# Optimization experiments

Measured on AMD Instinct MI355X. Metric: run time of the kernel, lower is better.

Reference implementation:

```python
import jax, jax.numpy as jnp
import numpy as np

NUM_HEADS = 16
NUM_GROUPS = 32  # min(C//4, 32) with C=1024
EPS = 1e-6       # flax GroupNorm default


def setup_inputs() -> dict:
    key = jax.random.key(0)
    ks = jax.random.split(key, 3)
    B, L, C = 2, 2048, 1024
    x = jax.random.normal(ks[0], (B, L, C), dtype=jnp.float32)
    gn_scale = jnp.ones((C,), jnp.float32)
    gn_bias = jnp.zeros((C,), jnp.float32)
    qkv_w = jax.random.normal(ks[1], (C, 3 * C), jnp.float32) * (C ** -0.5)
    qkv_b = jnp.zeros((3 * C,), jnp.float32)
    proj_w = jax.random.normal(ks[2], (C, C), jnp.float32) * 1e-5  # default_init(1e-10) ~ tiny
    proj_b = jnp.zeros((C,), jnp.float32)
    return {"x": x, "gn_scale": gn_scale, "gn_bias": gn_bias,
            "qkv_w": qkv_w, "qkv_b": qkv_b, "proj_w": proj_w, "proj_b": proj_b}


def reference(x, gn_scale, gn_bias, qkv_w, qkv_b, proj_w, proj_b):
    B, L, C = x.shape
    H = NUM_HEADS
    hd = C // H
    # GroupNorm over (L, channels-in-group)
    xg = x.reshape(B, L, NUM_GROUPS, C // NUM_GROUPS)
    mu = jnp.mean(xg, axis=(1, 3), keepdims=True)
    var = jnp.var(xg, axis=(1, 3), keepdims=True)
    xn = ((xg - mu) * jax.lax.rsqrt(var + EPS)).reshape(B, L, C)
    xn = xn * gn_scale + gn_bias
    # 1x1-conv QKV projection == dense
    qkv = xn @ qkv_w + qkv_b                       # [B, L, 3C]
    qkv = qkv.reshape(B, L, H, 3 * hd)             # interleaved per-head q|k|v
    q, k, v = jnp.split(qkv, 3, axis=-1)           # each [B, L, H, hd]
    scale = 1.0 / jnp.sqrt(hd)
    logits = jnp.einsum('btnh,bfnh->bnft', k, q * scale)  # [B, H, L, L]
    weights = jax.nn.softmax(logits, axis=-1)
    h = jnp.einsum('bnft,btnh->bfnh', weights, v).reshape(B, L, C)
    h = h @ proj_w + proj_b
    # CombineResidualSkip, project_skip=False
    return (x + h) / np.sqrt(2.0)
```

## Files before the change

kernel.cpp:

```cpp
#include <hip/hip_runtime.h>
#include <hip/hip_bf16.h>

typedef __hip_bfloat16 bf16;
typedef __attribute__((ext_vector_type(8))) __bf16 bf16x8;
typedef __attribute__((ext_vector_type(4))) float floatx4;

#define NB 2
#define NL 2048
#define NC 1024
#define NH 16
#define ND 64

__device__ __forceinline__ void async_copy16(void* lds, const void* g) {
  __builtin_amdgcn_global_load_lds(
      (__attribute__((address_space(1))) void*)(const_cast<void*>(g)),
      (__attribute__((address_space(3))) void*)(lds), 16, 0, 0);
}

__device__ __forceinline__ floatx4 mfma16(bf16x8 a, bf16x8 b, floatx4 c) {
  return __builtin_amdgcn_mfma_f32_16x16x32_bf16(a, b, c, 0, 0, 0);
}

__global__ __launch_bounds__(256) void gn_part_kernel(
    const float* __restrict__ x, float2* __restrict__ part) {
  int bg = blockIdx.x >> 3, sl = blockIdx.x & 7;
  int b = bg >> 5, g = bg & 31;
  const float* base = x + (size_t)b * NL * NC + (size_t)(sl * 256) * NC + g * 32;
  float s = 0.f, ss = 0.f;
  for (int vi = threadIdx.x; vi < 2048; vi += 256) {
    int l = vi >> 3, j = (vi & 7) * 4;
    float4 u = *(const float4*)(base + (size_t)l * NC + j);
    s += u.x + u.y + u.z + u.w;
    ss += u.x * u.x + u.y * u.y + u.z * u.z + u.w * u.w;
  }
  for (int off = 32; off; off >>= 1) {
    s += __shfl_down(s, off);
    ss += __shfl_down(ss, off);
  }
  __shared__ float rs[4], rss[4];
  int wave = threadIdx.x >> 6, lane = threadIdx.x & 63;
  if (lane == 0) { rs[wave] = s; rss[wave] = ss; }
  __syncthreads();
  if (threadIdx.x == 0) {
    part[blockIdx.x] = make_float2(rs[0] + rs[1] + rs[2] + rs[3],
                                   rss[0] + rss[1] + rss[2] + rss[3]);
  }
}

__global__ __launch_bounds__(256) void gn_apply_kernel(
    const float* __restrict__ x, const float2* __restrict__ part,
    const float* __restrict__ scale, const float* __restrict__ bias,
    bf16* __restrict__ xn) {
  size_t idx = (size_t)blockIdx.x * 256 + threadIdx.x;
  size_t e = idx * 8;
  int c = (int)(e & (NC - 1));
  int b = (int)(e >> 21);
  int bg = b * 32 + (c >> 5);
  float s = 0.f, ss = 0.f;
#pragma unroll
  for (int i = 0; i < 8; ++i) {
    float2 p = part[bg * 8 + i];
    s += p.x; ss += p.y;
  }
  float mean = s * (1.f / 65536.f);
  float var = ss * (1.f / 65536.f) - mean * mean;
  float rstd = rsqrtf(var + 1e-6f);
  float4 x0 = *(const float4*)(x + e);
  float4 x1 = *(const float4*)(x + e + 4);
  float4 s0 = *(const float4*)(scale + c);
  float4 s1 = *(const float4*)(scale + c + 4);
  float4 b0 = *(const float4*)(bias + c);
  float4 b1 = *(const float4*)(bias + c + 4);
  float xv[8] = {x0.x, x0.y, x0.z, x0.w, x1.x, x1.y, x1.z, x1.w};
  float sv[8] = {s0.x, s0.y, s0.z, s0.w, s1.x, s1.y, s1.z, s1.w};
  float bv[8] = {b0.x, b0.y, b0.z, b0.w, b1.x, b1.y, b1.z, b1.w};
  bf16 o[8];
#pragma unroll
  for (int k = 0; k < 8; ++k)
    o[k] = __float2bfloat16((xv[k] - mean) * rstd * sv[k] + bv[k]);
  *(uint4*)(xn + e) = *(const uint4*)o;
}

__global__ void transpose_f32_bf16(const float* __restrict__ in,
                                   bf16* __restrict__ out, int R, int C) {
  __shared__ float t[32][33];
  int c0 = blockIdx.x * 32, r0 = blockIdx.y * 32;
#pragma unroll
  for (int j = 0; j < 4; ++j)
    t[threadIdx.y + j * 8][threadIdx.x] =
        in[(size_t)(r0 + threadIdx.y + j * 8) * C + c0 + threadIdx.x];
  __syncthreads();
#pragma unroll
  for (int j = 0; j < 4; ++j)
    out[(size_t)(c0 + threadIdx.y + j * 8) * R + r0 + threadIdx.x] =
        __float2bfloat16(t[threadIdx.x][threadIdx.y + j * 8]);
}

template <int MODE, int NT>
__global__ __launch_bounds__(256) void gemm_kernel(
    const bf16* __restrict__ A, const bf16* __restrict__ Bt,
    const float* __restrict__ biasv, const float* __restrict__ xres,
    bf16* __restrict__ Qo, bf16* __restrict__ Ko, bf16* __restrict__ Vto,
    float* __restrict__ out, int M, int N, int K) {
  constexpr int NFR = NT / 32;
  __shared__ bf16 As[128 * 32];
  __shared__ bf16 Bs[NT * 32];
  int tid = threadIdx.x, wave = tid >> 6, lane = tid & 63;
  int col = lane & 15, quad = lane >> 4;
  int mB = blockIdx.y * 128, nB = blockIdx.x * NT;
  int wm = (wave >> 1) * 64, wn = (wave & 1) * (NT / 2);
  floatx4 acc[4][NFR];
#pragma unroll
  for (int i = 0; i < 4; ++i)
#pragma unroll
    for (int j = 0; j < NFR; ++j) acc[i][j] = (floatx4){0.f, 0.f, 0.f, 0.f};

  int rowOff = wave * 32 + (lane >> 2);
  int rowOffB = (NT == 128) ? rowOff : (wave * 16 + (lane >> 2));
  int kOff = (lane & 3) * 8;

  for (int k0 = 0; k0 < K; k0 += 32) {
    __syncthreads();
    const bf16* ga = A + (size_t)(mB + rowOff) * K + k0 + kOff;
    async_copy16(&As[(wave * 32) * 32], ga);
    async_copy16(&As[(wave * 32 + 16) * 32], ga + (size_t)16 * K);
    const bf16* gb = Bt + (size_t)(nB + rowOffB) * K + k0 + kOff;
    if (NT == 128) {
      async_copy16(&Bs[(wave * 32) * 32], gb);
      async_copy16(&Bs[(wave * 32 + 16) * 32], gb + (size_t)16 * K);
    } else {
      async_copy16(&Bs[(wave * 16) * 32], gb);
    }
    __syncthreads();
    bf16x8 af[4], bfr[NFR];
#pragma unroll
    for (int mi = 0; mi < 4; ++mi)
      af[mi] = *(const bf16x8*)&As[(wm + mi * 16 + col) * 32 + quad * 8];
#pragma unroll
    for (int ni = 0; ni < NFR; ++ni)
      bfr[ni] = *(const bf16x8*)&Bs[(wn + ni * 16 + col) * 32 + quad * 8];
#pragma unroll
    for (int mi = 0; mi < 4; ++mi)
#pragma unroll
      for (int ni = 0; ni < NFR; ++ni)
        acc[mi][ni] = mfma16(af[mi], bfr[ni], acc[mi][ni]);
  }

#pragma unroll
  for (int mi = 0; mi < 4; ++mi)
#pragma unroll
    for (int ni = 0; ni < NFR; ++ni)
#pragma unroll
      for (int r = 0; r < 4; ++r) {
        int row = mB + wm + mi * 16 + quad * 4 + r;
        int ncol = nB + wn + ni * 16 + col;
        float v = acc[mi][ni][r] + biasv[ncol];
        if (MODE == 0) {
          int b = row >> 11, f = row & 2047;
          int h = ncol / 192, rr = ncol - h * 192;
          size_t bhl = ((size_t)(b * NH + h) * NL + f);
          if (rr < 64)
            Qo[bhl * 64 + rr] = __float2bfloat16(v * 0.125f);
          else if (rr < 128)
            Ko[bhl * 64 + rr - 64] = __float2bfloat16(v);
          else
            Vto[((size_t)(b * NH + h) * 64 + (rr - 128)) * NL + f] = __float2bfloat16(v);
        } else {
          size_t o = (size_t)row * N + ncol;
          out[o] = (xres[o] + v) * 0.70710678118654752f;
        }
      }
}

__global__ __launch_bounds__(256, 3) void attn_kernel(
    const bf16* __restrict__ Q, const bf16* __restrict__ Kb,
    const bf16* __restrict__ Vt, bf16* __restrict__ hout) {
  int qt = blockIdx.x, bh = blockIdx.y;
  int b = bh >> 4, h = bh & 15;
  int tid = threadIdx.x, wave = tid >> 6, lane = tid & 63;
  int m = lane & 15, quad = lane >> 4;
  int tg = wave >> 1, th = wave & 1;

  __shared__ bf16 Kd[2][4096];
  __shared__ bf16 Vd[2][4096];
  __shared__ bf16 Pp[4][2048];

  bf16* Psw = Pp[wave];

  const bf16* Kg = Kb + (size_t)bh * NL * 64;
  const bf16* Vg = Vt + (size_t)bh * 64 * NL;

  bf16x8 bq[2][2];
  {
    const bf16* Qg = Q + ((size_t)bh * NL + qt * 64 + tg * 32) * 64;
#pragma unroll
    for (int nf = 0; nf < 2; ++nf)
#pragma unroll
      for (int c = 0; c < 2; ++c)
        bq[nf][c] = *(const bf16x8*)&Qg[(size_t)(nf * 16 + m) * 64 + c * 32 + quad * 8];
  }

  float lrow[2] = {0.f, 0.f};
  floatx4 o[2][4];
#pragma unroll
  for (int nf = 0; nf < 2; ++nf)
#pragma unroll
    for (int di = 0; di < 4; ++di) o[nf][di] = (floatx4){0.f, 0.f, 0.f, 0.f};

  int srow = lane >> 3, schunk = lane & 7;

  auto stage = [&](int bufi, int t0) {
#pragma unroll
    for (int i = 0; i < 2; ++i) {
      int r0 = wave * 16 + i * 8;
      int r = r0 + srow;
      int cg = schunk ^ (r & 7);
      async_copy16(&Kd[bufi][r0 * 64], Kg + (size_t)(t0 + r) * 64 + cg * 8);
      async_copy16(&Vd[bufi][r0 * 64], Vg + (size_t)r * NL + t0 + cg * 8);
    }
  };

  stage(0, 0);
  __syncthreads();

  int buf = 0;
  for (int t0 = 0; t0 < NL; t0 += 64) {
    if (t0 + 64 < NL) stage(buf ^ 1, t0 + 64);

    const bf16* Kbase = Kd[buf];
    const bf16* Vbase = Vd[buf];

    floatx4 s[2][2];
#pragma unroll
    for (int nf = 0; nf < 2; ++nf)
#pragma unroll
      for (int ti = 0; ti < 2; ++ti) s[nf][ti] = (floatx4){0.f, 0.f, 0.f, 0.f};
#pragma unroll
    for (int ti = 0; ti < 2; ++ti)
#pragma unroll
      for (int c = 0; c < 2; ++c) {
        bf16x8 ak = *(const bf16x8*)
            &Kbase[(th * 32 + ti * 16 + m) * 64 + ((c * 4 + quad) ^ (m & 7)) * 8];
        s[0][ti] = mfma16(ak, bq[0][c], s[0][ti]);
        s[1][ti] = mfma16(ak, bq[1][c], s[1][ti]);
      }

#pragma unroll
    for (int nf = 0; nf < 2; ++nf) {
      float ls = 0.f;
#pragma unroll
      for (int ti = 0; ti < 2; ++ti)
#pragma unroll
        for (int r = 0; r < 4; ++r) {
          float p = __expf(s[nf][ti][r]);
          s[nf][ti][r] = p;
          ls += p;
        }
      ls += __shfl_xor(ls, 16);
      ls += __shfl_xor(ls, 32);
      lrow[nf] += ls;
#pragma unroll
      for (int ti = 0; ti < 2; ++ti) {
        bf16 pk[4];
#pragma unroll
        for (int r = 0; r < 4; ++r) pk[r] = __float2bfloat16(s[nf][ti][r]);
        int ct = ti * 2 + (quad >> 1);
        *(uint2*)&Psw[(nf * 16 + m) * 64 + ((ct ^ (m & 7)) * 8) + (quad & 1) * 4] =
            *(const uint2*)pk;
      }
    }

    bf16x8 bp[2];
#pragma unroll
    for (int nf = 0; nf < 2; ++nf)
      bp[nf] = *(const bf16x8*)&Psw[(nf * 16 + m) * 64 + ((quad ^ (m & 7)) * 8)];
#pragma unroll
    for (int di = 0; di < 4; ++di) {
      bf16x8 av = *(const bf16x8*)
          &Vbase[(di * 16 + m) * 64 + ((th * 4 + quad) ^ (m & 7)) * 8];
      o[0][di] = mfma16(av, bp[0], o[0][di]);
      o[1][di] = mfma16(av, bp[1], o[1][di]);
    }

    __syncthreads();
    buf ^= 1;
  }

  float* So = (float*)Kd;
  float* Sl = (float*)Vd;
  if (th == 1) {
#pragma unroll
    for (int nf = 0; nf < 2; ++nf) {
      Sl[tg * 128 + nf * 64 + lane] = lrow[nf];
#pragma unroll
      for (int di = 0; di < 4; ++di)
#pragma unroll
        for (int r = 0; r < 4; ++r)
          So[tg * 2048 + (nf * 16 + di * 4 + r) * 64 + lane] = o[nf][di][r];
    }
  }
  __syncthreads();
  if (th == 0) {
#pragma unroll
    for (int nf = 0; nf < 2; ++nf) {
      lrow[nf] += Sl[tg * 128 + nf * 64 + lane];
#pragma unroll
      for (int di = 0; di < 4; ++di)
#pragma unroll
        for (int r = 0; r < 4; ++r)
          o[nf][di][r] += So[tg * 2048 + (nf * 16 + di * 4 + r) * 64 + lane];
    }
#pragma unroll
    for (int nf = 0; nf < 2; ++nf) {
      float rl = 1.f / lrow[nf];
      int l = qt * 64 + tg * 32 + nf * 16 + m;
      bf16* hp = hout + (size_t)(b * NL + l) * NC + h * 64;
#pragma unroll
      for (int di = 0; di < 4; ++di) {
        bf16 pk[4];
#pragma unroll
        for (int r = 0; r < 4; ++r) pk[r] = __float2bfloat16(o[nf][di][r] * rl);
        *(uint2*)&hp[di * 16 + quad * 4] = *(const uint2*)pk;
      }
    }
  }
}

extern "C" void kernel_launch(void* const* d_in, const int* in_sizes, int n_in,
                              void* d_out, int out_size, void* d_ws, size_t ws_size,
                              hipStream_t stream) {
  const float* x = (const float*)d_in[0];
  const float* gn_scale = (const float*)d_in[1];
  const float* gn_bias = (const float*)d_in[2];
  const float* qkv_w = (const float*)d_in[3];
  const float* qkv_b = (const float*)d_in[4];
  const float* proj_w = (const float*)d_in[5];
  const float* proj_b = (const float*)d_in[6];
  float* out = (float*)d_out;

  bf16* xn = (bf16*)d_out;

  char* ws = (char*)d_ws;
  float2* part = (float2*)ws;
  bf16* Qb = (bf16*)(ws + 4096);
  bf16* Kbuf = Qb + 4194304;
  bf16* Vt = Kbuf + 4194304;
  bf16* hat = Vt + 4194304;
  bf16* wqkvT = hat;
  bf16* projT = Qb;

  gn_part_kernel<<<512, 256, 0, stream>>>(x, part);
  gn_apply_kernel<<<2048, 256, 0, stream>>>(x, part, gn_scale, gn_bias, xn);
  transpose_f32_bf16<<<dim3(96, 32), dim3(32, 8), 0, stream>>>(qkv_w, wqkvT, 1024, 3072);
  gemm_kernel<0, 128><<<dim3(24, 32), 256, 0, stream>>>(
      xn, wqkvT, qkv_b, nullptr, Qb, Kbuf, Vt, nullptr, 4096, 3072, 1024);
  attn_kernel<<<dim3(32, 32), 256, 0, stream>>>(Qb, Kbuf, Vt, hat);
  transpose_f32_bf16<<<dim3(32, 32), dim3(32, 8), 0, stream>>>(proj_w, projT, 1024, 1024);
  gemm_kernel<1, 64><<<dim3(16, 32), 256, 0, stream>>>(
      hat, projT, proj_b, x, nullptr, nullptr, nullptr, out, 4096, 1024, 1024);
}
```

Before: 241.4 us.

## Enlarge attention blocks to 8 waves owning full key tiles per query slice

The attention kernel now uses 512-thread blocks covering 256 queries, with each wave handling 32 queries over the full 64-key tile instead of splitting keys between wave pairs. This removes the end-of-kernel LDS reduction of partial outputs and row sums. It also amortizes each staged K/V tile across twice as many waves, reducing global K/V reads. In exchange the grid shrinks to 256 blocks, which lowers occupancy and latency hiding, and the per-wave register footprint grows.

```diff
diff --git a/kernel.cpp b/kernel.cpp
--- a/kernel.cpp
+++ b/kernel.cpp
@@ -172,18 +172,17 @@
       }
 }
 
-__global__ __launch_bounds__(256, 3) void attn_kernel(
+__global__ __launch_bounds__(512, 2) void attn_kernel(
     const bf16* __restrict__ Q, const bf16* __restrict__ Kb,
     const bf16* __restrict__ Vt, bf16* __restrict__ hout) {
   int qt = blockIdx.x, bh = blockIdx.y;
   int b = bh >> 4, h = bh & 15;
   int tid = threadIdx.x, wave = tid >> 6, lane = tid & 63;
   int m = lane & 15, quad = lane >> 4;
-  int tg = wave >> 1, th = wave & 1;
 
   __shared__ bf16 Kd[2][4096];
   __shared__ bf16 Vd[2][4096];
-  __shared__ bf16 Pp[4][2048];
+  __shared__ bf16 Pp[8][2048];
 
   bf16* Psw = Pp[wave];
 
@@ -192,7 +191,7 @@
 
   bf16x8 bq[2][2];
   {
-    const bf16* Qg = Q + ((size_t)bh * NL + qt * 64 + tg * 32) * 64;
+    const bf16* Qg = Q + ((size_t)bh * NL + qt * 256 + wave * 32) * 64;
 #pragma unroll
     for (int nf = 0; nf < 2; ++nf)
 #pragma unroll
@@ -210,14 +209,11 @@
   int srow = lane >> 3, schunk = lane & 7;
 
   auto stage = [&](int bufi, int t0) {
-#pragma unroll
-    for (int i = 0; i < 2; ++i) {
-      int r0 = wave * 16 + i * 8;
-      int r = r0 + srow;
-      int cg = schunk ^ (r & 7);
-      async_copy16(&Kd[bufi][r0 * 64], Kg + (size_t)(t0 + r) * 64 + cg * 8);
-      async_copy16(&Vd[bufi][r0 * 64], Vg + (size_t)r * NL + t0 + cg * 8);
-    }
+    int r0 = wave * 8;
+    int r = r0 + srow;
+    int cg = schunk ^ (r & 7);
+    async_copy16(&Kd[bufi][r0 * 64], Kg + (size_t)(t0 + r) * 64 + cg * 8);
+    async_copy16(&Vd[bufi][r0 * 64], Vg + (size_t)r * NL + t0 + cg * 8);
   };
 
   stage(0, 0);
@@ -230,17 +226,17 @@
     const bf16* Kbase = Kd[buf];
     const bf16* Vbase = Vd[buf];
 
-    floatx4 s[2][2];
+    floatx4 s[2][4];
 #pragma unroll
     for (int nf = 0; nf < 2; ++nf)
 #pragma unroll
-      for (int ti = 0; ti < 2; ++ti) s[nf][ti] = (floatx4){0.f, 0.f, 0.f, 0.f};
-#pragma unroll
-    for (int ti = 0; ti < 2; ++ti)
+      for (int ti = 0; ti < 4; ++ti) s[nf][ti] = (floatx4){0.f, 0.f, 0.f, 0.f};
+#pragma unroll
+    for (int ti = 0; ti < 4; ++ti)
 #pragma unroll
       for (int c = 0; c < 2; ++c) {
         bf16x8 ak = *(const bf16x8*)
-            &Kbase[(th * 32 + ti * 16 + m) * 64 + ((c * 4 + quad) ^ (m & 7)) * 8];
+            &Kbase[(ti * 16 + m) * 64 + ((c * 4 + quad) ^ (m & 7)) * 8];
         s[0][ti] = mfma16(ak, bq[0][c], s[0][ti]);
         s[1][ti] = mfma16(ak, bq[1][c], s[1][ti]);
       }
@@ -249,7 +245,7 @@
     for (int nf = 0; nf < 2; ++nf) {
       float ls = 0.f;
 #pragma unroll
-      for (int ti = 0; ti < 2; ++ti)
+      for (int ti = 0; ti < 4; ++ti)
 #pragma unroll
         for (int r = 0; r < 4; ++r) {
           float p = __expf(s[nf][ti][r]);
@@ -260,7 +256,7 @@
       ls += __shfl_xor(ls, 32);
       lrow[nf] += ls;
 #pragma unroll
-      for (int ti = 0; ti < 2; ++ti) {
+      for (int ti = 0; ti < 4; ++ti) {
         bf16 pk[4];
 #pragma unroll
         for (int r = 0; r < 4; ++r) pk[r] = __float2bfloat16(s[nf][ti][r]);
@@ -270,58 +266,37 @@
       }
     }
 
-    bf16x8 bp[2];
-#pragma unroll
-    for (int nf = 0; nf < 2; ++nf)
-      bp[nf] = *(const bf16x8*)&Psw[(nf * 16 + m) * 64 + ((quad ^ (m & 7)) * 8)];
-#pragma unroll
-    for (int di = 0; di < 4; ++di) {
-      bf16x8 av = *(const bf16x8*)
-          &Vbase[(di * 16 + m) * 64 + ((th * 4 + quad) ^ (m & 7)) * 8];
-      o[0][di] = mfma16(av, bp[0], o[0][di]);
-      o[1][di] = mfma16(av, bp[1], o[1][di]);
+#pragma unroll
+    for (int c = 0; c < 2; ++c) {
+      bf16x8 bp[2];
+#pragma unroll
+      for (int nf = 0; nf < 2; ++nf)
+        bp[nf] = *(const bf16x8*)
+            &Psw[(nf * 16 + m) * 64 + (((c * 4 + quad) ^ (m & 7)) * 8)];
+#pragma unroll
+      for (int di = 0; di < 4; ++di) {
+        bf16x8 av = *(const bf16x8*)
+            &Vbase[(di * 16 + m) * 64 + ((c * 4 + quad) ^ (m & 7)) * 8];
+        o[0][di] = mfma16(av, bp[0], o[0][di]);
+        o[1][di] = mfma16(av, bp[1], o[1][di]);
+      }
     }
 
     __syncthreads();
     buf ^= 1;
   }
 
-  float* So = (float*)Kd;
-  float* Sl = (float*)Vd;
-  if (th == 1) {
-#pragma unroll
-    for (int nf = 0; nf < 2; ++nf) {
-      Sl[tg * 128 + nf * 64 + lane] = lrow[nf];
-#pragma unroll
-      for (int di = 0; di < 4; ++di)
-#pragma unroll
-        for (int r = 0; r < 4; ++r)
-          So[tg * 2048 + (nf * 16 + di * 4 + r) * 64 + lane] = o[nf][di][r];
-    }
-  }
-  __syncthreads();
-  if (th == 0) {
-#pragma unroll
-    for (int nf = 0; nf < 2; ++nf) {
-      lrow[nf] += Sl[tg * 128 + nf * 64 + lane];
-#pragma unroll
-      for (int di = 0; di < 4; ++di)
-#pragma unroll
-        for (int r = 0; r < 4; ++r)
-          o[nf][di][r] += So[tg * 2048 + (nf * 16 + di * 4 + r) * 64 + lane];
-    }
-#pragma unroll
-    for (int nf = 0; nf < 2; ++nf) {
-      float rl = 1.f / lrow[nf];
-      int l = qt * 64 + tg * 32 + nf * 16 + m;
-      bf16* hp = hout + (size_t)(b * NL + l) * NC + h * 64;
-#pragma unroll
-      for (int di = 0; di < 4; ++di) {
-        bf16 pk[4];
-#pragma unroll
-        for (int r = 0; r < 4; ++r) pk[r] = __float2bfloat16(o[nf][di][r] * rl);
-        *(uint2*)&hp[di * 16 + quad * 4] = *(const uint2*)pk;
-      }
+#pragma unroll
+  for (int nf = 0; nf < 2; ++nf) {
+    float rl = 1.f / lrow[nf];
+    int l = qt * 256 + wave * 32 + nf * 16 + m;
+    bf16* hp = hout + (size_t)(b * NL + l) * NC + h * 64;
+#pragma unroll
+    for (int di = 0; di < 4; ++di) {
+      bf16 pk[4];
+#pragma unroll
+      for (int r = 0; r < 4; ++r) pk[r] = __float2bfloat16(o[nf][di][r] * rl);
+      *(uint2*)&hp[di * 16 + quad * 4] = *(const uint2*)pk;
     }
   }
 }
@@ -354,7 +329,7 @@
   transpose_f32_bf16<<<dim3(96, 32), dim3(32, 8), 0, stream>>>(qkv_w, wqkvT, 1024, 3072);
   gemm_kernel<0, 128><<<dim3(24, 32), 256, 0, stream>>>(
       xn, wqkvT, qkv_b, nullptr, Qb, Kbuf, Vt, nullptr, 4096, 3072, 1024);
-  attn_kernel<<<dim3(32, 32), 256, 0, stream>>>(Qb, Kbuf, Vt, hat);
+  attn_kernel<<<dim3(8, 32), 512, 0, stream>>>(Qb, Kbuf, Vt, hat);
   transpose_f32_bf16<<<dim3(32, 32), dim3(32, 8), 0, stream>>>(proj_w, projT, 1024, 1024);
   gemm_kernel<1, 64><<<dim3(16, 32), 256, 0, stream>>>(
       hat, projT, proj_b, x, nullptr, nullptr, nullptr, out, 4096, 1024, 1024);
```

Result: faster. 218.2 us (-9.6%).
